# Optimization experiments

Measured on AMD Instinct MI355X. Metric: run time of the kernel, lower is better.

## Reference

```python
import jax, jax.numpy as jnp
import numpy as np

TEMPERATURE_INIT = 0.1
EPS_NORM = 1e-12   # torch F.normalize eps
EPS_LOG = 1e-08


def _l2_normalize(x, axis=-1):
    n = jnp.linalg.norm(x, axis=axis, keepdims=True)
    return x / jnp.maximum(n, EPS_NORM)


def setup_inputs() -> dict:
    key = jax.random.key(0)
    k1, k2, k3, k4 = jax.random.split(key, 4)
    B, D = 8192, 1024
    z_rna = jax.random.uniform(k1, (B, D), dtype=jnp.float32)
    z_atac = jax.random.uniform(k2, (B, D), dtype=jnp.float32)
    link_matrix = jax.random.uniform(k3, (D, D), dtype=jnp.float32)
    temp_param = jax.random.uniform(k4, (), dtype=jnp.float32)
    return {"z_rna": z_rna, "z_atac": z_atac, "link_matrix": link_matrix,
            "temp_param": temp_param}


def reference(z_rna, z_atac, link_matrix, temp_param):
    # link matrix is row-L2-normalized in __init__
    link = _l2_normalize(link_matrix, axis=-1)           # (D, D)
    rn = _l2_normalize(z_rna, axis=-1)                   # (B, D)
    an = _l2_normalize(z_atac, axis=-1)                  # (B, D)
    # sum_ij link_ij * rn_bi * an_bj  == rn . (link @ an^T per-row)
    # algebraically identical to the torch (B,D,D) broadcast reduction
    cos_sim = jnp.einsum('bi,ij,bj->b', rn, link, an)    # (B,)
    # adaptive temperature from mean embedding entropy
    ent_rna = -jnp.sum(rn * jnp.log(rn + EPS_LOG), axis=-1).mean()
    ent_atac = -jnp.sum(an * jnp.log(an + EPS_LOG), axis=-1).mean()
    avg_entropy = (ent_rna + ent_atac) / 2
    s = jax.nn.sigmoid(temp_param)
    adaptive_scale = s * TEMPERATURE_INIT + (1.0 - s) * avg_entropy
    tau = jnp.clip(adaptive_scale, 0.01, 1.0)
    loss = -jnp.mean(cos_sim / tau)
    return loss
```

## Files before the change

### kernel.cpp

```cpp
#include <hip/hip_runtime.h>
#include <hip/hip_bf16.h>

#define BD 8192
#define DD 1024
#define BM 128
#define BN 128
#define BKK 64

typedef __attribute__((ext_vector_type(8))) short short8;
typedef __attribute__((ext_vector_type(4))) float floatx4;

__device__ inline float bf2f(unsigned short u) {
    union { unsigned int u; float f; } un;
    un.u = ((unsigned int)u) << 16;
    return un.f;
}
__device__ inline unsigned short f2bf(float f) {
    union { float f; unsigned int u; } un;
    un.f = f;
    unsigned int u = un.u;
    u += 0x7FFF + ((u >> 16) & 1);
    return (unsigned short)(u >> 16);
}

__device__ inline void gld_lds16(const void* g, void* l) {
    __builtin_amdgcn_global_load_lds(
        (const __attribute__((address_space(1))) unsigned int*)g,
        (__attribute__((address_space(3))) unsigned int*)l, 16, 0, 0);
}

template <bool ENT>
__global__ __launch_bounds__(256) void norm_wave(const float* __restrict__ x,
                                                 unsigned short* __restrict__ xb,
                                                 float* __restrict__ ent_part,
                                                 int nrows) {
    int lane = threadIdx.x & 63;
    int wid = threadIdx.x >> 6;
    int gw = blockIdx.x * 4 + wid;
    int nw = gridDim.x * 4;
    float epart = 0.f;
    for (int row = gw; row < nrows; row += nw) {
        const float4* xr = (const float4*)(x + (size_t)row * DD);
        float4 v0 = xr[lane];
        float4 v1 = xr[lane + 64];
        float4 v2 = xr[lane + 128];
        float4 v3 = xr[lane + 192];
        float ss = v0.x*v0.x + v0.y*v0.y + v0.z*v0.z + v0.w*v0.w
                 + v1.x*v1.x + v1.y*v1.y + v1.z*v1.z + v1.w*v1.w
                 + v2.x*v2.x + v2.y*v2.y + v2.z*v2.z + v2.w*v2.w
                 + v3.x*v3.x + v3.y*v3.y + v3.z*v3.z + v3.w*v3.w;
#pragma unroll
        for (int off = 1; off < 64; off <<= 1) ss += __shfl_xor(ss, off);
        float inv = 1.0f / fmaxf(sqrtf(ss), 1e-12f);
        ushort4* orow = (ushort4*)(xb + (size_t)row * DD);
        float4 vv[4] = {v0, v1, v2, v3};
#pragma unroll
        for (int i = 0; i < 4; ++i) {
            float a = vv[i].x * inv, b = vv[i].y * inv, c = vv[i].z * inv, d = vv[i].w * inv;
            ushort4 o;
            o.x = f2bf(a); o.y = f2bf(b); o.z = f2bf(c); o.w = f2bf(d);
            orow[lane + 64 * i] = o;
            if (ENT) {
                epart += a * __logf(a + 1e-8f) + b * __logf(b + 1e-8f)
                       + c * __logf(c + 1e-8f) + d * __logf(d + 1e-8f);
            }
        }
    }
    if (ENT) {
#pragma unroll
        for (int off = 1; off < 64; off <<= 1) epart += __shfl_xor(epart, off);
        __shared__ float sw[4];
        if (lane == 0) sw[wid] = epart;
        __syncthreads();
        if (threadIdx.x == 0) ent_part[blockIdx.x] = sw[0] + sw[1] + sw[2] + sw[3];
    }
}

__global__ __launch_bounds__(256) void gemm_cos(const unsigned short* __restrict__ anb,
                                                const unsigned short* __restrict__ linkb,
                                                const unsigned short* __restrict__ rnb,
                                                float* __restrict__ cos_partial) {
    __shared__ unsigned short As[BM * BKK];
    __shared__ unsigned short Bs[BN * BKK];

    int bid = blockIdx.x;
    int j = bid >> 3;
    int btile = (bid & 7) * 8 + (j & 7);
    int itile = j >> 3;
    int b0 = btile * BM;
    int i0 = itile * BN;

    int tid = threadIdx.x;
    int wid = tid >> 6, lane = tid & 63;
    int wm = wid >> 1, wn = wid & 1;
    int r = lane & 15, kg = lane >> 4;

    int srow = tid >> 3;
    int scb = (tid & 7) * 16;
    int scb_src = scb ^ ((srow & 7) << 4);

    const char* agbase = (const char*)anb + ((size_t)(b0 + srow) * DD) * 2 + scb_src;
    const char* bgbase = (const char*)linkb + ((size_t)(i0 + srow) * DD) * 2 + scb_src;
    unsigned short* al = As + srow * BKK + scb / 2;
    unsigned short* bl = Bs + srow * BKK + scb / 2;

    floatx4 acc[4][4];
#pragma unroll
    for (int m = 0; m < 4; ++m)
#pragma unroll
        for (int n = 0; n < 4; ++n) acc[m][n] = (floatx4)0.0f;

#pragma unroll
    for (int c = 0; c < 4; ++c) {
        gld_lds16(agbase + (size_t)c * 32 * DD * 2, al + c * 2048);
        gld_lds16(bgbase + (size_t)c * 32 * DD * 2, bl + c * 2048);
    }

    for (int k0 = 0; k0 < DD; k0 += BKK) {
        __syncthreads();
#pragma unroll
        for (int kk = 0; kk < 2; ++kk) {
            short8 a_[4], b_[4];
#pragma unroll
            for (int m = 0; m < 4; ++m) {
                int row = wm * 64 + m * 16 + r;
                int cb = (kg * 16 + kk * 64) ^ ((row & 7) << 4);
                a_[m] = *(const short8*)((const char*)As + row * 128 + cb);
            }
#pragma unroll
            for (int n = 0; n < 4; ++n) {
                int row = wn * 64 + n * 16 + r;
                int cb = (kg * 16 + kk * 64) ^ ((row & 7) << 4);
                b_[n] = *(const short8*)((const char*)Bs + row * 128 + cb);
            }
#pragma unroll
            for (int m = 0; m < 4; ++m)
#pragma unroll
                for (int n = 0; n < 4; ++n)
                    acc[m][n] = __builtin_amdgcn_mfma_f32_16x16x32_bf16(a_[m], b_[n], acc[m][n], 0, 0, 0);
        }
        __syncthreads();
        if (k0 + BKK < DD) {
            size_t kb = (size_t)(k0 + BKK) * 2;
#pragma unroll
            for (int c = 0; c < 4; ++c) {
                gld_lds16(agbase + (size_t)c * 32 * DD * 2 + kb, al + c * 2048);
                gld_lds16(bgbase + (size_t)c * 32 * DD * 2 + kb, bl + c * 2048);
            }
        }
    }

    int b0w = b0 + wm * 64, i0w = i0 + wn * 64;
#pragma unroll
    for (int m = 0; m < 4; ++m) {
#pragma unroll
        for (int rr = 0; rr < 4; ++rr) {
            int bb = b0w + m * 16 + kg * 4 + rr;
            float p = 0.f;
#pragma unroll
            for (int n = 0; n < 4; ++n) {
                int ii = i0w + n * 16 + r;
                p += acc[m][n][rr] * bf2f(rnb[(size_t)bb * DD + ii]);
            }
#pragma unroll
            for (int off = 1; off < 16; off <<= 1) p += __shfl_xor(p, off);
            if (r == 0) atomicAdd(&cos_partial[bb], p);
        }
    }
}

__global__ __launch_bounds__(256) void finalize(const float* __restrict__ cos_partial,
                                                const float* __restrict__ er,
                                                const float* __restrict__ ea,
                                                const float* __restrict__ temp,
                                                float* __restrict__ out) {
    __shared__ float sb[4][3];
    float s = 0.f, se = 0.f, sa = 0.f;
    for (int i = threadIdx.x; i < BD; i += 256) s += cos_partial[i];
    for (int i = threadIdx.x; i < 1024; i += 256) { se += er[i]; sa += ea[i]; }
#pragma unroll
    for (int off = 1; off < 64; off <<= 1) {
        s += __shfl_xor(s, off);
        se += __shfl_xor(se, off);
        sa += __shfl_xor(sa, off);
    }
    int wid = threadIdx.x >> 6, lane = threadIdx.x & 63;
    if (lane == 0) { sb[wid][0] = s; sb[wid][1] = se; sb[wid][2] = sa; }
    __syncthreads();
    if (threadIdx.x == 0) {
        float total = sb[0][0] + sb[1][0] + sb[2][0] + sb[3][0];
        float ser = sb[0][1] + sb[1][1] + sb[2][1] + sb[3][1];
        float sea = sb[0][2] + sb[1][2] + sb[2][2] + sb[3][2];
        float ent_rna = -ser / (float)BD;
        float ent_atac = -sea / (float)BD;
        float avg = 0.5f * (ent_rna + ent_atac);
        float t = temp[0];
        float sg = 1.0f / (1.0f + __expf(-t));
        float scale = sg * 0.1f + (1.0f - sg) * avg;
        float tau = fminf(fmaxf(scale, 0.01f), 1.0f);
        out[0] = -(total / (float)BD) / tau;
    }
}

extern "C" void kernel_launch(void* const* d_in, const int* in_sizes, int n_in,
                              void* d_out, int out_size, void* d_ws, size_t ws_size,
                              hipStream_t stream) {
    const float* z_rna = (const float*)d_in[0];
    const float* z_atac = (const float*)d_in[1];
    const float* link = (const float*)d_in[2];
    const float* temp = (const float*)d_in[3];
    float* out = (float*)d_out;

    char* ws = (char*)d_ws;
    float* cos_partial = (float*)ws;
    float* er_part = (float*)(ws + 32768);
    float* ea_part = (float*)(ws + 36864);
    unsigned short* linkb = (unsigned short*)(ws + 40960);
    unsigned short* rnb = (unsigned short*)(ws + 40960 + 2097152);
    unsigned short* anb = (unsigned short*)(ws + 40960 + 2097152 + 16777216);

    hipMemsetAsync(d_ws, 0, 40960, stream);
    norm_wave<false><<<256, 256, 0, stream>>>(link, linkb, nullptr, DD);
    norm_wave<true><<<1024, 256, 0, stream>>>(z_rna, rnb, er_part, BD);
    norm_wave<true><<<1024, 256, 0, stream>>>(z_atac, anb, ea_part, BD);
    gemm_cos<<<512, 256, 0, stream>>>(anb, linkb, rnb, cos_partial);
    finalize<<<1, 256, 0, stream>>>(cos_partial, er_part, ea_part, temp, out);
}
```

Baseline: 149.9 us.

## Fuse normalization launches, split-K GEMM, and replace per-row atomics with block partials

```diff
diff --git a/kernel.cpp b/kernel.cpp
--- a/kernel.cpp
+++ b/kernel.cpp
@@ -29,66 +29,76 @@
         (__attribute__((address_space(3))) unsigned int*)l, 16, 0, 0);
 }
 
-template <bool ENT>
-__global__ __launch_bounds__(256) void norm_wave(const float* __restrict__ x,
-                                                 unsigned short* __restrict__ xb,
-                                                 float* __restrict__ ent_part,
-                                                 int nrows) {
-    int lane = threadIdx.x & 63;
-    int wid = threadIdx.x >> 6;
-    int gw = blockIdx.x * 4 + wid;
-    int nw = gridDim.x * 4;
+__global__ __launch_bounds__(256) void norm_all(const float* __restrict__ rna,
+                                                const float* __restrict__ atac,
+                                                const float* __restrict__ link,
+                                                unsigned short* __restrict__ rnb,
+                                                unsigned short* __restrict__ anb,
+                                                unsigned short* __restrict__ linkb,
+                                                float* __restrict__ er,
+                                                float* __restrict__ ea) {
+    int bid = blockIdx.x;
+    int wid = threadIdx.x >> 6, lane = threadIdx.x & 63;
+    const float* x;
+    unsigned short* xb;
+    float* ep;
+    int row;
+    bool ent = true;
+    if (bid < 2048)      { x = rna;  xb = rnb;   ep = er + bid;          row = bid * 4 + wid; }
+    else if (bid < 4096) { x = atac; xb = anb;   ep = ea + (bid - 2048); row = (bid - 2048) * 4 + wid; }
+    else                 { x = link; xb = linkb; ep = nullptr;           row = (bid - 4096) * 4 + wid; ent = false; }
+
+    const float4* xr = (const float4*)(x + (size_t)row * DD);
+    float4 v0 = xr[lane];
+    float4 v1 = xr[lane + 64];
+    float4 v2 = xr[lane + 128];
+    float4 v3 = xr[lane + 192];
+    float ss = v0.x*v0.x + v0.y*v0.y + v0.z*v0.z + v0.w*v0.w
+             + v1.x*v1.x + v1.y*v1.y + v1.z*v1.z + v1.w*v1.w
+             + v2.x*v2.x + v2.y*v2.y + v2.z*v2.z + v2.w*v2.w
+             + v3.x*v3.x + v3.y*v3.y + v3.z*v3.z + v3.w*v3.w;
+#pragma unroll
+    for (int off = 1; off < 64; off <<= 1) ss += __shfl_xor(ss, off);
+    float inv = 1.0f / fmaxf(sqrtf(ss), 1e-12f);
+    ushort4* orow = (ushort4*)(xb + (size_t)row * DD);
+    float4 vv[4] = {v0, v1, v2, v3};
     float epart = 0.f;
-    for (int row = gw; row < nrows; row += nw) {
-        const float4* xr = (const float4*)(x + (size_t)row * DD);
-        float4 v0 = xr[lane];
-        float4 v1 = xr[lane + 64];
-        float4 v2 = xr[lane + 128];
-        float4 v3 = xr[lane + 192];
-        float ss = v0.x*v0.x + v0.y*v0.y + v0.z*v0.z + v0.w*v0.w
-                 + v1.x*v1.x + v1.y*v1.y + v1.z*v1.z + v1.w*v1.w
-                 + v2.x*v2.x + v2.y*v2.y + v2.z*v2.z + v2.w*v2.w
-                 + v3.x*v3.x + v3.y*v3.y + v3.z*v3.z + v3.w*v3.w;
-#pragma unroll
-        for (int off = 1; off < 64; off <<= 1) ss += __shfl_xor(ss, off);
-        float inv = 1.0f / fmaxf(sqrtf(ss), 1e-12f);
-        ushort4* orow = (ushort4*)(xb + (size_t)row * DD);
-        float4 vv[4] = {v0, v1, v2, v3};
-#pragma unroll
-        for (int i = 0; i < 4; ++i) {
-            float a = vv[i].x * inv, b = vv[i].y * inv, c = vv[i].z * inv, d = vv[i].w * inv;
-            ushort4 o;
-            o.x = f2bf(a); o.y = f2bf(b); o.z = f2bf(c); o.w = f2bf(d);
-            orow[lane + 64 * i] = o;
-            if (ENT) {
-                epart += a * __logf(a + 1e-8f) + b * __logf(b + 1e-8f)
-                       + c * __logf(c + 1e-8f) + d * __logf(d + 1e-8f);
-            }
-        }
-    }
-    if (ENT) {
+#pragma unroll
+    for (int i = 0; i < 4; ++i) {
+        float a = vv[i].x * inv, b = vv[i].y * inv, c = vv[i].z * inv, d = vv[i].w * inv;
+        ushort4 o;
+        o.x = f2bf(a); o.y = f2bf(b); o.z = f2bf(c); o.w = f2bf(d);
+        orow[lane + 64 * i] = o;
+        if (ent) {
+            epart += a * __logf(a + 1e-8f) + b * __logf(b + 1e-8f)
+                   + c * __logf(c + 1e-8f) + d * __logf(d + 1e-8f);
+        }
+    }
+    if (ent) {
 #pragma unroll
         for (int off = 1; off < 64; off <<= 1) epart += __shfl_xor(epart, off);
         __shared__ float sw[4];
         if (lane == 0) sw[wid] = epart;
         __syncthreads();
-        if (threadIdx.x == 0) ent_part[blockIdx.x] = sw[0] + sw[1] + sw[2] + sw[3];
+        if (threadIdx.x == 0) ep[0] = sw[0] + sw[1] + sw[2] + sw[3];
     }
 }
 
 __global__ __launch_bounds__(256) void gemm_cos(const unsigned short* __restrict__ anb,
                                                 const unsigned short* __restrict__ linkb,
                                                 const unsigned short* __restrict__ rnb,
-                                                float* __restrict__ cos_partial) {
+                                                float* __restrict__ gpart) {
     __shared__ unsigned short As[BM * BKK];
     __shared__ unsigned short Bs[BN * BKK];
 
     int bid = blockIdx.x;
     int j = bid >> 3;
     int btile = (bid & 7) * 8 + (j & 7);
-    int itile = j >> 3;
+    int itile = (j >> 3) & 7;
+    int ks = j >> 6;
     int b0 = btile * BM;
     int i0 = itile * BN;
+    int kbase = ks * 512;
 
     int tid = threadIdx.x;
     int wid = tid >> 6, lane = tid & 63;
@@ -99,8 +109,8 @@
     int scb = (tid & 7) * 16;
     int scb_src = scb ^ ((srow & 7) << 4);
 
-    const char* agbase = (const char*)anb + ((size_t)(b0 + srow) * DD) * 2 + scb_src;
-    const char* bgbase = (const char*)linkb + ((size_t)(i0 + srow) * DD) * 2 + scb_src;
+    const char* agbase = (const char*)anb + ((size_t)(b0 + srow) * DD + kbase) * 2 + scb_src;
+    const char* bgbase = (const char*)linkb + ((size_t)(i0 + srow) * DD + kbase) * 2 + scb_src;
     unsigned short* al = As + srow * BKK + scb / 2;
     unsigned short* bl = Bs + srow * BKK + scb / 2;
 
@@ -116,7 +126,7 @@
         gld_lds16(bgbase + (size_t)c * 32 * DD * 2, bl + c * 2048);
     }
 
-    for (int k0 = 0; k0 < DD; k0 += BKK) {
+    for (int step = 0; step < 8; ++step) {
         __syncthreads();
 #pragma unroll
         for (int kk = 0; kk < 2; ++kk) {
@@ -140,8 +150,8 @@
                     acc[m][n] = __builtin_amdgcn_mfma_f32_16x16x32_bf16(a_[m], b_[n], acc[m][n], 0, 0, 0);
         }
         __syncthreads();
-        if (k0 + BKK < DD) {
-            size_t kb = (size_t)(k0 + BKK) * 2;
+        if (step < 7) {
+            size_t kb = (size_t)(step + 1) * BKK * 2;
 #pragma unroll
             for (int c = 0; c < 4; ++c) {
                 gld_lds16(agbase + (size_t)c * 32 * DD * 2 + kb, al + c * 2048);
@@ -151,33 +161,34 @@
     }
 
     int b0w = b0 + wm * 64, i0w = i0 + wn * 64;
+    float s = 0.f;
 #pragma unroll
     for (int m = 0; m < 4; ++m) {
 #pragma unroll
         for (int rr = 0; rr < 4; ++rr) {
-            int bb = b0w + m * 16 + kg * 4 + rr;
-            float p = 0.f;
-#pragma unroll
-            for (int n = 0; n < 4; ++n) {
-                int ii = i0w + n * 16 + r;
-                p += acc[m][n][rr] * bf2f(rnb[(size_t)bb * DD + ii]);
-            }
-#pragma unroll
-            for (int off = 1; off < 16; off <<= 1) p += __shfl_xor(p, off);
-            if (r == 0) atomicAdd(&cos_partial[bb], p);
-        }
-    }
-}
-
-__global__ __launch_bounds__(256) void finalize(const float* __restrict__ cos_partial,
+            const unsigned short* rrow = rnb + (size_t)(b0w + m * 16 + kg * 4 + rr) * DD + i0w + r;
+#pragma unroll
+            for (int n = 0; n < 4; ++n)
+                s += acc[m][n][rr] * bf2f(rrow[n * 16]);
+        }
+    }
+#pragma unroll
+    for (int off = 1; off < 64; off <<= 1) s += __shfl_xor(s, off);
+    __shared__ float sw[4];
+    if (lane == 0) sw[wid] = s;
+    __syncthreads();
+    if (tid == 0) gpart[blockIdx.x] = sw[0] + sw[1] + sw[2] + sw[3];
+}
+
+__global__ __launch_bounds__(256) void finalize(const float* __restrict__ gpart,
                                                 const float* __restrict__ er,
                                                 const float* __restrict__ ea,
                                                 const float* __restrict__ temp,
                                                 float* __restrict__ out) {
     __shared__ float sb[4][3];
     float s = 0.f, se = 0.f, sa = 0.f;
-    for (int i = threadIdx.x; i < BD; i += 256) s += cos_partial[i];
-    for (int i = threadIdx.x; i < 1024; i += 256) { se += er[i]; sa += ea[i]; }
+    for (int i = threadIdx.x; i < 1024; i += 256) s += gpart[i];
+    for (int i = threadIdx.x; i < 2048; i += 256) { se += er[i]; sa += ea[i]; }
 #pragma unroll
     for (int off = 1; off < 64; off <<= 1) {
         s += __shfl_xor(s, off);
@@ -212,17 +223,14 @@
     float* out = (float*)d_out;
 
     char* ws = (char*)d_ws;
-    float* cos_partial = (float*)ws;
-    float* er_part = (float*)(ws + 32768);
-    float* ea_part = (float*)(ws + 36864);
-    unsigned short* linkb = (unsigned short*)(ws + 40960);
-    unsigned short* rnb = (unsigned short*)(ws + 40960 + 2097152);
-    unsigned short* anb = (unsigned short*)(ws + 40960 + 2097152 + 16777216);
-
-    hipMemsetAsync(d_ws, 0, 40960, stream);
-    norm_wave<false><<<256, 256, 0, stream>>>(link, linkb, nullptr, DD);
-    norm_wave<true><<<1024, 256, 0, stream>>>(z_rna, rnb, er_part, BD);
-    norm_wave<true><<<1024, 256, 0, stream>>>(z_atac, anb, ea_part, BD);
-    gemm_cos<<<512, 256, 0, stream>>>(anb, linkb, rnb, cos_partial);
-    finalize<<<1, 256, 0, stream>>>(cos_partial, er_part, ea_part, temp, out);
-}
+    float* gpart = (float*)ws;
+    float* er_part = (float*)(ws + 4096);
+    float* ea_part = (float*)(ws + 12288);
+    unsigned short* linkb = (unsigned short*)(ws + 32768);
+    unsigned short* rnb = (unsigned short*)(ws + 32768 + 2097152);
+    unsigned short* anb = (unsigned short*)(ws + 32768 + 2097152 + 16777216);
+
+    norm_all<<<4352, 256, 0, stream>>>(z_rna, z_atac, link, rnb, anb, linkb, er_part, ea_part);
+    gemm_cos<<<1024, 256, 0, stream>>>(anb, linkb, rnb, gpart);
+    finalize<<<1, 256, 0, stream>>>(gpart, er_part, ea_part, temp, out);
+}
```

Result: faster. 129.4 us (-13.7%).
